# Kernel optimization log

Hardware: AMD Instinct MI355X
Metric: run time of the kernel (lower is better)

## Reference

```python
import jax, jax.numpy as jnp
import numpy as np

NUM_PRIMARY_CAPS = 32
PRIMARY_CAP_DIM = 8
CLASS_CAP_DIM = 16
NUM_SLOTS = 100
ROUTING_ITERS = 3
PRIOR_STRENGTH = 0.1
PRIOR_DECAY = 0.02
TEMPERATURE_INIT = 30.0

INPUT_DIM = 20000
NUM_LABELS = 100
BATCH = 4096


def _layernorm(x, g, b, eps=1e-5):
    mu = x.mean(axis=-1, keepdims=True)
    var = x.var(axis=-1, keepdims=True)
    return (x - mu) / jnp.sqrt(var + eps) * g + b


def _squash(t, axis=-1):
    sq = (t ** 2).sum(axis=axis, keepdims=True)
    scale = sq / (1.0 + sq)
    return scale * t / jnp.sqrt(sq + 1e-8)


def _l2norm(x, axis=-1, eps=1e-12):
    n = jnp.sqrt((x ** 2).sum(axis=axis, keepdims=True))
    return x / jnp.maximum(n, eps)


def setup_inputs() -> dict:
    key = jax.random.key(0)
    ks = jax.random.split(key, 12)
    features = jax.random.normal(ks[0], (BATCH, INPUT_DIM), dtype=jnp.float32)
    features = _l2norm(features)  # L2-normalised TF-IDF per docstring
    slot_features = jax.random.normal(ks[1], (BATCH, NUM_SLOTS), dtype=jnp.float32)
    # embedding MLP: Linear(input_dim,512) ReLU Linear(512,256) ReLU LayerNorm(256)
    W1 = jax.random.normal(ks[2], (INPUT_DIM, 512), dtype=jnp.float32) * 0.02
    b1 = jnp.zeros((512,), jnp.float32)
    W2 = jax.random.normal(ks[3], (512, 256), dtype=jnp.float32) * 0.05
    b2 = jnp.zeros((256,), jnp.float32)
    ln_g = jnp.ones((256,), jnp.float32)
    ln_b = jnp.zeros((256,), jnp.float32)
    # primary caps: 32 independent Linear(256,8)+LayerNorm(8), stacked
    pc_W = jax.random.normal(ks[4], (NUM_PRIMARY_CAPS, 256, PRIMARY_CAP_DIM), dtype=jnp.float32) * 0.06
    pc_b = jnp.zeros((NUM_PRIMARY_CAPS, PRIMARY_CAP_DIM), jnp.float32)
    pc_g = jnp.ones((NUM_PRIMARY_CAPS, PRIMARY_CAP_DIM), jnp.float32)
    pc_beta = jnp.zeros((NUM_PRIMARY_CAPS, PRIMARY_CAP_DIM), jnp.float32)
    # digit caps routing weights [N, K, out, in] * 0.1 per torch init
    dc_W = jax.random.normal(ks[5], (NUM_PRIMARY_CAPS, NUM_LABELS, CLASS_CAP_DIM, PRIMARY_CAP_DIM), dtype=jnp.float32) * 0.1
    slot_priors = jax.random.normal(ks[6], (NUM_SLOTS, NUM_LABELS), dtype=jnp.float32) * 0.05
    targets = _l2norm(jax.random.normal(ks[7], (NUM_LABELS, CLASS_CAP_DIM), dtype=jnp.float32))
    temperature = jnp.asarray(TEMPERATURE_INIT, dtype=jnp.float32)
    return {"features": features, "slot_features": slot_features,
            "W1": W1, "b1": b1, "W2": W2, "b2": b2, "ln_g": ln_g, "ln_b": ln_b,
            "pc_W": pc_W, "pc_b": pc_b, "pc_g": pc_g, "pc_beta": pc_beta,
            "dc_W": dc_W, "slot_priors": slot_priors, "targets": targets,
            "temperature": temperature}


def reference(features, slot_features, W1, b1, W2, b2, ln_g, ln_b,
              pc_W, pc_b, pc_g, pc_beta, dc_W, slot_priors, targets, temperature):
    # embedding MLP (dropout is identity at inference)
    h = jax.nn.relu(features @ W1 + b1)
    h = jax.nn.relu(h @ W2 + b2)
    h = _layernorm(h, ln_g, ln_b)                      # [B, 256]
    # primary capsules: [B, N=32, 8]
    prim = jnp.einsum('bc,ncd->bnd', h, pc_W) + pc_b[None]
    prim = _layernorm(prim, pc_g[None], pc_beta[None])
    # routing predictions: [B, N, K, out]
    predictions = jnp.einsum('bni,njoi->bnjo', prim, dc_W)
    B = features.shape[0]
    # slot prior: relu -> normalize to simplex -> center -> project to classes
    sf_relu = jax.nn.relu(slot_features)
    sf_w = sf_relu / jnp.maximum(sf_relu.sum(axis=1, keepdims=True), 1e-6)
    sf_w = sf_w - 1.0 / NUM_SLOTS
    sp = (sf_w @ slot_priors)[:, None, :, None]        # [B, 1, K, 1]
    b = jnp.zeros((B, NUM_PRIMARY_CAPS, predictions.shape[2], 1), predictions.dtype)
    b = b + sp * PRIOR_STRENGTH
    v = None
    for i in range(ROUTING_ITERS):
        c = jax.nn.softmax(b, axis=2)                  # coupling coefficients
        s = (predictions * c).sum(axis=1, keepdims=True)
        v = _squash(s, axis=-1)                        # [B, 1, K, out]
        if i < ROUTING_ITERS - 1:
            b = b + (predictions * v).sum(axis=-1, keepdims=True)
            strength_i = max(0.0, PRIOR_STRENGTH - PRIOR_DECAY * (i + 1))
            b = b + sp * strength_i
    class_caps = v[:, 0]                               # [B, K, out]
    caps_n = _l2norm(class_caps)
    logits = (caps_n * targets[None]).sum(axis=-1) * temperature
    return logits
```

## Files before the change

kernel.cpp:

```cpp
#include <hip/hip_runtime.h>
#include <hip/hip_bf16.h>

#define B_SZ   4096
#define NPC    32
#define NJ     100
#define CD     16
#define PD     8

typedef float  f32x4  __attribute__((ext_vector_type(4)));
typedef __bf16 bf16x8 __attribute__((ext_vector_type(8)));

__device__ __forceinline__ unsigned short f2bfr(float f) {
    union { float f; unsigned u; } v; v.f = f;
    return (unsigned short)((v.u + 0x8000u) >> 16);
}
__device__ __forceinline__ float bf_lo(unsigned u) {
    union { unsigned u; float f; } v; v.u = u << 16; return v.f;
}
__device__ __forceinline__ float bf_hi(unsigned u) {
    union { unsigned u; float f; } v; v.u = u & 0xffff0000u; return v.f;
}

__global__ __launch_bounds__(256) void transpose_cvt(
    const float* __restrict__ W, unsigned short* __restrict__ out)
{
    __shared__ float tile[32][33];
    const int kb = blockIdx.x * 32;
    const int nb = blockIdx.y * 32;
    const int tx = threadIdx.x & 31, ty = threadIdx.x >> 5;
#pragma unroll
    for (int i = 0; i < 4; ++i)
        tile[ty + 8 * i][tx] = W[(size_t)(kb + ty + 8 * i) * 512 + nb + tx];
    __syncthreads();
#pragma unroll
    for (int i = 0; i < 4; ++i)
        out[(size_t)(nb + ty + 8 * i) * 20000 + kb + tx] = f2bfr(tile[tx][ty + 8 * i]);
}

__global__ __launch_bounds__(256) void gemm1_mfma(
    const float* __restrict__ A,
    const unsigned short* __restrict__ Bt,
    float* __restrict__ C)
{
    __shared__ __align__(16) unsigned short As[128 * 32];
    __shared__ __align__(16) unsigned short Bs[128 * 32];
    const int t = threadIdx.x;
    const int lane = t & 63, w = t >> 6;
    const int id = blockIdx.x;
    const int m0 = (id & 31) * 128;
    const int n0 = ((id >> 5) & 3) * 128;
    const int z  = id >> 7;

    const int srow = t >> 2, skc = t & 3;
    const float*          Ap  = A  + (size_t)(m0 + srow) * 20000 + z * 4000 + skc * 8;
    const float*          Ap2 = Ap + (size_t)64 * 20000;
    const unsigned short* Bp  = Bt + (size_t)(n0 + srow) * 20000 + z * 4000 + skc * 8;
    const unsigned short* Bp2 = Bp + (size_t)64 * 20000;

    const int wr = w >> 1, wc = w & 1;
    const int fr = lane & 15, fq = lane >> 4;

    f32x4 acc[4][4] = {};

    for (int kt = 0; kt < 125; ++kt) {
        const int k0 = kt * 32;
        float4 a0 = *(const float4*)(Ap  + k0);
        float4 a1 = *(const float4*)(Ap  + k0 + 4);
        float4 a2 = *(const float4*)(Ap2 + k0);
        float4 a3 = *(const float4*)(Ap2 + k0 + 4);
        uint4  q0 = *(const uint4*)(Bp  + k0);
        uint4  q1 = *(const uint4*)(Bp2 + k0);
        uint4 p0, p1;
        p0.x = (unsigned)f2bfr(a0.x) | ((unsigned)f2bfr(a0.y) << 16);
        p0.y = (unsigned)f2bfr(a0.z) | ((unsigned)f2bfr(a0.w) << 16);
        p0.z = (unsigned)f2bfr(a1.x) | ((unsigned)f2bfr(a1.y) << 16);
        p0.w = (unsigned)f2bfr(a1.z) | ((unsigned)f2bfr(a1.w) << 16);
        p1.x = (unsigned)f2bfr(a2.x) | ((unsigned)f2bfr(a2.y) << 16);
        p1.y = (unsigned)f2bfr(a2.z) | ((unsigned)f2bfr(a2.w) << 16);
        p1.z = (unsigned)f2bfr(a3.x) | ((unsigned)f2bfr(a3.y) << 16);
        p1.w = (unsigned)f2bfr(a3.z) | ((unsigned)f2bfr(a3.w) << 16);
        *(uint4*)(As + (size_t)t * 8)         = p0;
        *(uint4*)(As + (size_t)(t + 256) * 8) = p1;
        *(uint4*)(Bs + (size_t)t * 8)         = q0;
        *(uint4*)(Bs + (size_t)(t + 256) * 8) = q1;
        __syncthreads();
        bf16x8 af[4], bg[4];
#pragma unroll
        for (int mi = 0; mi < 4; ++mi)
            af[mi] = *(const bf16x8*)(As + (size_t)((wr * 64 + mi * 16 + fr) * 32 + fq * 8));
#pragma unroll
        for (int ni = 0; ni < 4; ++ni)
            bg[ni] = *(const bf16x8*)(Bs + (size_t)((wc * 64 + ni * 16 + fr) * 32 + fq * 8));
#pragma unroll
        for (int mi = 0; mi < 4; ++mi)
#pragma unroll
            for (int ni = 0; ni < 4; ++ni)
                acc[mi][ni] = __builtin_amdgcn_mfma_f32_16x16x32_bf16(
                    af[mi], bg[ni], acc[mi][ni], 0, 0, 0);
        __syncthreads();
    }

    const int er = fq * 4, ec = fr;
#pragma unroll
    for (int mi = 0; mi < 4; ++mi)
#pragma unroll
    for (int ni = 0; ni < 4; ++ni) {
        const size_t base = (size_t)(m0 + wr * 64 + mi * 16 + er) * 512
                          + n0 + wc * 64 + ni * 16 + ec;
#pragma unroll
        for (int r = 0; r < 4; ++r)
            atomicAdd(&C[base + (size_t)r * 512], acc[mi][ni][r]);
    }
}

__global__ __launch_bounds__(256) void gemm2_fused(
    const float* __restrict__ A, const float* __restrict__ b1v,
    const float* __restrict__ Bm, const float* __restrict__ bias,
    float* __restrict__ C, int M, int N, int K)
{
    __shared__ float As[16][68];
    __shared__ float Bs[16][64];
    const int t  = threadIdx.x;
    const int tx = t & 15, ty = t >> 4;
    const int m0 = blockIdx.y * 64, n0 = blockIdx.x * 64;

    const int arow = t >> 2;
    const int ak   = (t & 3) << 2;
    const int bk   = t >> 4;
    const int bn   = (t & 15) << 2;

    const float* Aptr = A + (size_t)(m0 + arow) * K + ak;
    const float* Bptr = Bm + (size_t)bk * N + n0 + bn;

    float acc[4][4] = {};

    for (int k0 = 0; k0 < K; k0 += 16) {
        float4 av  = *(const float4*)(Aptr + k0);
        float4 b1q = *(const float4*)(b1v + k0 + ak);
        av.x = fmaxf(av.x + b1q.x, 0.f);
        av.y = fmaxf(av.y + b1q.y, 0.f);
        av.z = fmaxf(av.z + b1q.z, 0.f);
        av.w = fmaxf(av.w + b1q.w, 0.f);
        float4 bv = *(const float4*)(Bptr + (size_t)k0 * N);
        As[ak + 0][arow] = av.x;
        As[ak + 1][arow] = av.y;
        As[ak + 2][arow] = av.z;
        As[ak + 3][arow] = av.w;
        *(float4*)&Bs[bk][bn] = bv;
        __syncthreads();
#pragma unroll
        for (int kk = 0; kk < 16; ++kk) {
            float4 a = *(const float4*)&As[kk][ty << 2];
            float4 b = *(const float4*)&Bs[kk][tx << 2];
            acc[0][0] += a.x * b.x; acc[0][1] += a.x * b.y; acc[0][2] += a.x * b.z; acc[0][3] += a.x * b.w;
            acc[1][0] += a.y * b.x; acc[1][1] += a.y * b.y; acc[1][2] += a.y * b.z; acc[1][3] += a.y * b.w;
            acc[2][0] += a.z * b.x; acc[2][1] += a.z * b.y; acc[2][2] += a.z * b.z; acc[2][3] += a.z * b.w;
            acc[3][0] += a.w * b.x; acc[3][1] += a.w * b.y; acc[3][2] += a.w * b.z; acc[3][3] += a.w * b.w;
        }
        __syncthreads();
    }

    float4 bb = *(const float4*)(bias + n0 + (tx << 2));
#pragma unroll
    for (int i = 0; i < 4; ++i) {
        size_t m = (size_t)m0 + (ty << 2) + i;
        float4 o;
        o.x = fmaxf(acc[i][0] + bb.x, 0.f);
        o.y = fmaxf(acc[i][1] + bb.y, 0.f);
        o.z = fmaxf(acc[i][2] + bb.z, 0.f);
        o.w = fmaxf(acc[i][3] + bb.w, 0.f);
        *(float4*)(C + m * N + n0 + (tx << 2)) = o;
    }
}

__global__ __launch_bounds__(256) void layernorm256(
    const float* __restrict__ x, const float* __restrict__ g,
    const float* __restrict__ bta, float* __restrict__ y)
{
    const int w = threadIdx.x >> 6, lane = threadIdx.x & 63;
    const size_t row = (size_t)blockIdx.x * 4 + w;
    const float* xr = x + row * 256;
    float4 v = *(const float4*)(xr + lane * 4);
    float s  = v.x + v.y + v.z + v.w;
    float s2 = v.x * v.x + v.y * v.y + v.z * v.z + v.w * v.w;
#pragma unroll
    for (int off = 32; off; off >>= 1) {
        s  += __shfl_down(s, off);
        s2 += __shfl_down(s2, off);
    }
    s  = __shfl(s, 0);
    s2 = __shfl(s2, 0);
    float mu   = s * (1.f / 256.f);
    float var  = s2 * (1.f / 256.f) - mu * mu;
    float rstd = rsqrtf(var + 1e-5f);
    float4 gg = *(const float4*)(g + lane * 4);
    float4 bb = *(const float4*)(bta + lane * 4);
    float4 o;
    o.x = (v.x - mu) * rstd * gg.x + bb.x;
    o.y = (v.y - mu) * rstd * gg.y + bb.y;
    o.z = (v.z - mu) * rstd * gg.z + bb.z;
    o.w = (v.w - mu) * rstd * gg.w + bb.w;
    *(float4*)(y + row * 256 + lane * 4) = o;
}

__global__ __launch_bounds__(256) void prim_caps(
    const float* __restrict__ h, const float* __restrict__ pcW,
    const float* __restrict__ pcB, const float* __restrict__ pcG,
    const float* __restrict__ pcBeta, float* __restrict__ prim)
{
    __shared__ float hs[256];
    __shared__ float tmp[256];
    const int t = threadIdx.x;
    const size_t b = blockIdx.x;
    hs[t] = h[b * 256 + t];
    __syncthreads();
    const int n = t >> 3, d = t & 7;
    const float* wp = pcW + n * 256 * 8 + d;
    float acc = pcB[t];
#pragma unroll 4
    for (int k = 0; k < 256; ++k) acc += hs[k] * wp[k * 8];
    tmp[t] = acc;
    __syncthreads();
    float mu = 0.f, s2 = 0.f;
    const int base = n << 3;
#pragma unroll
    for (int q = 0; q < 8; ++q) {
        float xx = tmp[base + q];
        mu += xx;
        s2 += xx * xx;
    }
    mu *= 0.125f;
    s2 = s2 * 0.125f - mu * mu;
    float rstd = rsqrtf(s2 + 1e-5f);
    prim[b * 256 + t] = (acc - mu) * rstd * pcG[t] + pcBeta[t];
}

__global__ __launch_bounds__(1024, 4) void routing_b1(
    const float* __restrict__ prim,
    const float* __restrict__ sf,
    const float* __restrict__ priors,
    const float* __restrict__ dcW,
    const float* __restrict__ targets,
    const float* __restrict__ temp_p,
    float* __restrict__ out)
{
    __shared__ float    prim1[256];
    __shared__ unsigned predp[NPC * NJ * 9];
    __shared__ float    bst[NPC * NJ];
    __shared__ float    cst[NPC * NJ];
    __shared__ float    svv[NJ * 18];
    __shared__ float    spv[NJ];
    __shared__ float    rmv[NPC], irsv[NPC];
    __shared__ float    red[512];
    __shared__ float    red2[400];
    __shared__ float    ssum;

    const int t = threadIdx.x;
    const int lane = t & 63, w = t >> 6;

    const size_t b = blockIdx.x;

    if (t < 256) prim1[t] = prim[b * 256 + t];
    if (t < 128) red[t] = (t < 100) ? fmaxf(sf[b * 100 + t], 0.f) : 0.f;
    __syncthreads();

    if (t < 128) {
        float v = red[t];
#pragma unroll
        for (int d = 32; d; d >>= 1) v += __shfl_xor(v, d);
        if (lane == 0) red[128 + w] = v;
    }
    __syncthreads();
    if (t == 0) ssum = fmaxf(red[128] + red[129], 1e-6f);
    __syncthreads();

    if (t < 400) {
        const int j = t % 100, q = t / 100;
        const float inv = 1.f / ssum;
        float acc = 0.f;
#pragma unroll 5
        for (int k = q * 25; k < q * 25 + 25; ++k)
            acc += (red[k] * inv - 0.01f) * priors[k * 100 + j];
        red2[t] = acc;
    }
    __syncthreads();
    if (t < 100) spv[t] = red2[t] + red2[100 + t] + red2[200 + t] + red2[300 + t];
    __syncthreads();

    for (int r = t; r < NPC * NJ; r += 1024) bst[r] = spv[r % 100] * 0.1f;

    {
        const int c32 = lane & 31;
        const int hw  = t >> 5;
        const int ih  = (c32 & 1) * 4;
#pragma unroll 4
        for (int iter = 0; iter < 100; ++iter) {
            const int p = iter * 32 + hw;
            const int n = p / 100;
            const float4 wv = *(const float4*)(dcW + (size_t)p * 128 + c32 * 4);
            const float* pb = &prim1[n * 8 + ih];
            float part = wv.x * pb[0] + wv.y * pb[1] + wv.z * pb[2] + wv.w * pb[3];
            float po  = part + __shfl_xor(part, 1);
            float po2 = __shfl_xor(po, 2);
            if ((c32 & 3) == 0)
                predp[p * 9 + (c32 >> 2)] =
                    (unsigned)f2bfr(po) | ((unsigned)f2bfr(po2) << 16);
        }
    }
    __syncthreads();

    for (int it = 0; it < 3; ++it) {
        {
            const int n = t >> 5, q = t & 31;
            float mx = -1e30f;
            for (int j = q; j < 100; j += 32) mx = fmaxf(mx, bst[n * 100 + j]);
#pragma unroll
            for (int d = 1; d < 32; d <<= 1) mx = fmaxf(mx, __shfl_xor(mx, d));
            float se = 0.f;
            for (int j = q; j < 100; j += 32) se += __expf(bst[n * 100 + j] - mx);
#pragma unroll
            for (int d = 1; d < 32; d <<= 1) se += __shfl_xor(se, d);
            if (q == 0) { rmv[n] = mx; irsv[n] = 1.f / se; }
        }
        __syncthreads();
        for (int r = t; r < NPC * NJ; r += 1024)
            cst[r] = __expf(bst[r] - rmv[r / 100]) * irsv[r / 100];
        __syncthreads();

        if (t < 800) {
            const int j = t >> 3, op = t & 7;
            float s0 = 0.f, s1 = 0.f;
#pragma unroll
            for (int n = 0; n < NPC; ++n) {
                const float c = cst[n * 100 + j];
                const unsigned pk = predp[(n * 100 + j) * 9 + op];
                s0 += c * bf_lo(pk);
                s1 += c * bf_hi(pk);
            }
            float sq = s0 * s0 + s1 * s1;
            sq += __shfl_xor(sq, 1);
            sq += __shfl_xor(sq, 2);
            sq += __shfl_xor(sq, 4);
            const float fv = (sq / (1.f + sq)) / sqrtf(sq + 1e-8f);
            svv[j * 18 + op * 2]     = fv * s0;
            svv[j * 18 + op * 2 + 1] = fv * s1;
        }
        __syncthreads();

        if (it < 2) {
            const float str = 0.1f - 0.02f * (float)(it + 1);
            for (int r = t; r < NPC * NJ; r += 1024) {
                const int j = r % 100;
                float a = 0.f;
#pragma unroll
                for (int op = 0; op < 8; ++op) {
                    const unsigned pk = predp[r * 9 + op];
                    const float2 vv = *(const float2*)&svv[j * 18 + op * 2];
                    a += bf_lo(pk) * vv.x + bf_hi(pk) * vv.y;
                }
                bst[r] += a + spv[j] * str;
            }
            __syncthreads();
        }
    }

    if (t < 100) {
        const float T = *temp_p;
        float sq = 0.f, lg = 0.f;
#pragma unroll
        for (int o = 0; o < CD; ++o) {
            const float v = svv[t * 18 + o];
            sq += v * v;
            lg += v * targets[t * CD + o];
        }
        out[b * 100 + t] = lg * T / fmaxf(sqrtf(sq), 1e-12f);
    }
}

extern "C" void kernel_launch(void* const* d_in, const int* in_sizes, int n_in,
                              void* d_out, int out_size, void* d_ws, size_t ws_size,
                              hipStream_t stream)
{
    const float* features      = (const float*)d_in[0];
    const float* slot_features = (const float*)d_in[1];
    const float* W1            = (const float*)d_in[2];
    const float* b1            = (const float*)d_in[3];
    const float* W2            = (const float*)d_in[4];
    const float* b2            = (const float*)d_in[5];
    const float* ln_g          = (const float*)d_in[6];
    const float* ln_b          = (const float*)d_in[7];
    const float* pc_W          = (const float*)d_in[8];
    const float* pc_b          = (const float*)d_in[9];
    const float* pc_g          = (const float*)d_in[10];
    const float* pc_beta       = (const float*)d_in[11];
    const float* dc_W          = (const float*)d_in[12];
    const float* slot_priors   = (const float*)d_in[13];
    const float* targets       = (const float*)d_in[14];
    const float* temperature   = (const float*)d_in[15];
    float* out = (float*)d_out;

    unsigned short* Bt = (unsigned short*)d_ws;
    float* h1 = (float*)((char*)d_ws + (size_t)512 * 20000 * 2);
    float* h2 = h1 + (size_t)B_SZ * 512;
    float* h  = h2 + (size_t)B_SZ * 256;
    float* pr = h  + (size_t)B_SZ * 256;

    hipMemsetAsync(h1, 0, (size_t)B_SZ * 512 * sizeof(float), stream);

    transpose_cvt<<<dim3(625, 16), 256, 0, stream>>>(W1, Bt);
    gemm1_mfma<<<640, 256, 0, stream>>>(features, Bt, h1);
    gemm2_fused<<<dim3(256 / 64, B_SZ / 64), 256, 0, stream>>>(
        h1, b1, W2, b2, h2, B_SZ, 256, 512);
    layernorm256<<<B_SZ / 4, 256, 0, stream>>>(h2, ln_g, ln_b, h);
    prim_caps<<<B_SZ, 256, 0, stream>>>(h, pc_W, pc_b, pc_g, pc_beta, pr);
    routing_b1<<<B_SZ, 1024, 0, stream>>>(
        pr, slot_features, slot_priors, dc_W, targets, temperature, out);
}
```

Baseline: 1.362 ms.

## Reshape GEMM1 tiles to 64x256 and pre-convert routing weights to bf16

GEMM1 blocks change from 128x128 to 64x256 output tiles. Each block now converts only 64 fp32 rows of the large feature matrix to bf16 per K step, and the 512 output columns are covered by 2 column tiles instead of 4. That cuts how often each fp32 feature row is read and converted, at the cost of more bf16 weight traffic per block. Separately, the digit-capsule routing weights are converted once to bf16 in a new small kernel. The routing prediction loop then reads half as many bytes per batch element, with 16 threads per prediction group and fewer shuffles, which adds a small extra rounding in the weights.

```diff
diff --git a/kernel.cpp b/kernel.cpp
--- a/kernel.cpp
+++ b/kernel.cpp
@@ -37,60 +37,68 @@
         out[(size_t)(nb + ty + 8 * i) * 20000 + kb + tx] = f2bfr(tile[tx][ty + 8 * i]);
 }
 
+__global__ __launch_bounds__(256) void cvt_dcw(
+    const float* __restrict__ W, unsigned short* __restrict__ out)
+{
+    const size_t i = ((size_t)blockIdx.x * 256 + threadIdx.x) * 8;
+    float4 f0 = *(const float4*)(W + i);
+    float4 f1 = *(const float4*)(W + i + 4);
+    uint4 o;
+    o.x = (unsigned)f2bfr(f0.x) | ((unsigned)f2bfr(f0.y) << 16);
+    o.y = (unsigned)f2bfr(f0.z) | ((unsigned)f2bfr(f0.w) << 16);
+    o.z = (unsigned)f2bfr(f1.x) | ((unsigned)f2bfr(f1.y) << 16);
+    o.w = (unsigned)f2bfr(f1.z) | ((unsigned)f2bfr(f1.w) << 16);
+    *(uint4*)(out + i) = o;
+}
+
 __global__ __launch_bounds__(256) void gemm1_mfma(
     const float* __restrict__ A,
     const unsigned short* __restrict__ Bt,
     float* __restrict__ C)
 {
-    __shared__ __align__(16) unsigned short As[128 * 32];
-    __shared__ __align__(16) unsigned short Bs[128 * 32];
+    __shared__ __align__(16) unsigned short As[64 * 32];
+    __shared__ __align__(16) unsigned short Bs[256 * 32];
     const int t = threadIdx.x;
     const int lane = t & 63, w = t >> 6;
     const int id = blockIdx.x;
-    const int m0 = (id & 31) * 128;
-    const int n0 = ((id >> 5) & 3) * 128;
+    const int m0 = (id & 63) * 64;
+    const int n0 = ((id >> 6) & 1) * 256;
     const int z  = id >> 7;
 
     const int srow = t >> 2, skc = t & 3;
     const float*          Ap  = A  + (size_t)(m0 + srow) * 20000 + z * 4000 + skc * 8;
-    const float*          Ap2 = Ap + (size_t)64 * 20000;
     const unsigned short* Bp  = Bt + (size_t)(n0 + srow) * 20000 + z * 4000 + skc * 8;
-    const unsigned short* Bp2 = Bp + (size_t)64 * 20000;
-
-    const int wr = w >> 1, wc = w & 1;
+
     const int fr = lane & 15, fq = lane >> 4;
 
     f32x4 acc[4][4] = {};
 
     for (int kt = 0; kt < 125; ++kt) {
         const int k0 = kt * 32;
-        float4 a0 = *(const float4*)(Ap  + k0);
-        float4 a1 = *(const float4*)(Ap  + k0 + 4);
-        float4 a2 = *(const float4*)(Ap2 + k0);
-        float4 a3 = *(const float4*)(Ap2 + k0 + 4);
-        uint4  q0 = *(const uint4*)(Bp  + k0);
-        uint4  q1 = *(const uint4*)(Bp2 + k0);
-        uint4 p0, p1;
+        float4 a0 = *(const float4*)(Ap + k0);
+        float4 a1 = *(const float4*)(Ap + k0 + 4);
+        uint4  q0 = *(const uint4*)(Bp + k0);
+        uint4  q1 = *(const uint4*)(Bp + (size_t)64  * 20000 + k0);
+        uint4  q2 = *(const uint4*)(Bp + (size_t)128 * 20000 + k0);
+        uint4  q3 = *(const uint4*)(Bp + (size_t)192 * 20000 + k0);
+        uint4 p0;
         p0.x = (unsigned)f2bfr(a0.x) | ((unsigned)f2bfr(a0.y) << 16);
         p0.y = (unsigned)f2bfr(a0.z) | ((unsigned)f2bfr(a0.w) << 16);
         p0.z = (unsigned)f2bfr(a1.x) | ((unsigned)f2bfr(a1.y) << 16);
         p0.w = (unsigned)f2bfr(a1.z) | ((unsigned)f2bfr(a1.w) << 16);
-        p1.x = (unsigned)f2bfr(a2.x) | ((unsigned)f2bfr(a2.y) << 16);
-        p1.y = (unsigned)f2bfr(a2.z) | ((unsigned)f2bfr(a2.w) << 16);
-        p1.z = (unsigned)f2bfr(a3.x) | ((unsigned)f2bfr(a3.y) << 16);
-        p1.w = (unsigned)f2bfr(a3.z) | ((unsigned)f2bfr(a3.w) << 16);
         *(uint4*)(As + (size_t)t * 8)         = p0;
-        *(uint4*)(As + (size_t)(t + 256) * 8) = p1;
         *(uint4*)(Bs + (size_t)t * 8)         = q0;
         *(uint4*)(Bs + (size_t)(t + 256) * 8) = q1;
+        *(uint4*)(Bs + (size_t)(t + 512) * 8) = q2;
+        *(uint4*)(Bs + (size_t)(t + 768) * 8) = q3;
         __syncthreads();
         bf16x8 af[4], bg[4];
 #pragma unroll
         for (int mi = 0; mi < 4; ++mi)
-            af[mi] = *(const bf16x8*)(As + (size_t)((wr * 64 + mi * 16 + fr) * 32 + fq * 8));
+            af[mi] = *(const bf16x8*)(As + (size_t)((mi * 16 + fr) * 32 + fq * 8));
 #pragma unroll
         for (int ni = 0; ni < 4; ++ni)
-            bg[ni] = *(const bf16x8*)(Bs + (size_t)((wc * 64 + ni * 16 + fr) * 32 + fq * 8));
+            bg[ni] = *(const bf16x8*)(Bs + (size_t)((w * 64 + ni * 16 + fr) * 32 + fq * 8));
 #pragma unroll
         for (int mi = 0; mi < 4; ++mi)
 #pragma unroll
@@ -105,8 +113,8 @@
     for (int mi = 0; mi < 4; ++mi)
 #pragma unroll
     for (int ni = 0; ni < 4; ++ni) {
-        const size_t base = (size_t)(m0 + wr * 64 + mi * 16 + er) * 512
-                          + n0 + wc * 64 + ni * 16 + ec;
+        const size_t base = (size_t)(m0 + mi * 16 + er) * 512
+                          + n0 + w * 64 + ni * 16 + ec;
 #pragma unroll
         for (int r = 0; r < 4; ++r)
             atomicAdd(&C[base + (size_t)r * 512], acc[mi][ni][r]);
@@ -239,12 +247,12 @@
     const float* __restrict__ prim,
     const float* __restrict__ sf,
     const float* __restrict__ priors,
-    const float* __restrict__ dcW,
+    const unsigned short* __restrict__ dcWb,
     const float* __restrict__ targets,
     const float* __restrict__ temp_p,
     float* __restrict__ out)
 {
-    __shared__ float    prim1[256];
+    __shared__ __align__(16) float prim1[256];
     __shared__ unsigned predp[NPC * NJ * 9];
     __shared__ float    bst[NPC * NJ];
     __shared__ float    cst[NPC * NJ];
@@ -290,20 +298,23 @@
     for (int r = t; r < NPC * NJ; r += 1024) bst[r] = spv[r % 100] * 0.1f;
 
     {
-        const int c32 = lane & 31;
-        const int hw  = t >> 5;
-        const int ih  = (c32 & 1) * 4;
-#pragma unroll 4
-        for (int iter = 0; iter < 100; ++iter) {
-            const int p = iter * 32 + hw;
+        const int g = t >> 4;
+        const int o = t & 15;
+        const unsigned short* wp0 = dcWb + (size_t)g * 128 + o * 8;
+#pragma unroll 2
+        for (int iter = 0; iter < 50; ++iter) {
+            const int p = iter * 64 + g;
             const int n = p / 100;
-            const float4 wv = *(const float4*)(dcW + (size_t)p * 128 + c32 * 4);
-            const float* pb = &prim1[n * 8 + ih];
-            float part = wv.x * pb[0] + wv.y * pb[1] + wv.z * pb[2] + wv.w * pb[3];
-            float po  = part + __shfl_xor(part, 1);
-            float po2 = __shfl_xor(po, 2);
-            if ((c32 & 3) == 0)
-                predp[p * 9 + (c32 >> 2)] =
+            const uint4 wq = *(const uint4*)(wp0 + (size_t)iter * 8192);
+            const float4 pa = *(const float4*)&prim1[n * 8];
+            const float4 pb = *(const float4*)&prim1[n * 8 + 4];
+            float po = bf_lo(wq.x) * pa.x + bf_hi(wq.x) * pa.y
+                     + bf_lo(wq.y) * pa.z + bf_hi(wq.y) * pa.w
+                     + bf_lo(wq.z) * pb.x + bf_hi(wq.z) * pb.y
+                     + bf_lo(wq.w) * pb.z + bf_hi(wq.w) * pb.w;
+            const float po2 = __shfl_xor(po, 1);
+            if ((o & 1) == 0)
+                predp[p * 9 + (o >> 1)] =
                     (unsigned)f2bfr(po) | ((unsigned)f2bfr(po2) << 16);
         }
     }
@@ -404,15 +415,17 @@
     float* h2 = h1 + (size_t)B_SZ * 512;
     float* h  = h2 + (size_t)B_SZ * 256;
     float* pr = h  + (size_t)B_SZ * 256;
+    unsigned short* dcWb = (unsigned short*)(pr + (size_t)B_SZ * 256);
 
     hipMemsetAsync(h1, 0, (size_t)B_SZ * 512 * sizeof(float), stream);
 
     transpose_cvt<<<dim3(625, 16), 256, 0, stream>>>(W1, Bt);
+    cvt_dcw<<<200, 256, 0, stream>>>(dc_W, dcWb);
     gemm1_mfma<<<640, 256, 0, stream>>>(features, Bt, h1);
     gemm2_fused<<<dim3(256 / 64, B_SZ / 64), 256, 0, stream>>>(
         h1, b1, W2, b2, h2, B_SZ, 256, 512);
     layernorm256<<<B_SZ / 4, 256, 0, stream>>>(h2, ln_g, ln_b, h);
     prim_caps<<<B_SZ, 256, 0, stream>>>(h, pc_W, pc_b, pc_g, pc_beta, pr);
     routing_b1<<<B_SZ, 1024, 0, stream>>>(
-        pr, slot_features, slot_priors, dc_W, targets, temperature, out);
-}
+        pr, slot_features, slot_priors, dcWb, targets, temperature, out);
+}
```

After: 1.212 ms. 11.1% less time.
